# Kernel optimization log

Measured on AMD Instinct MI355X. Metric: run time of the kernel, lower is better.

The kernel has to match this reference:

```python
import jax, jax.numpy as jnp
import numpy as np

N_QUBITS = 13
DEPTH = 4
DIM = 2 ** N_QUBITS
PI = 3.141592653589793

# qubit 0 = most significant bit of the basis-state index
_idx = np.arange(DIM)
BITS = np.stack([(_idx >> (N_QUBITS - 1 - q)) & 1 for q in range(N_QUBITS)], axis=1)  # (DIM, n)
SIGNS = jnp.asarray(1.0 - 2.0 * BITS, dtype=jnp.float32)                               # Z eigenvalues, (DIM, n)
PARITY = jnp.asarray((-1.0) ** BITS.sum(axis=1), dtype=jnp.float32)                    # <Z^{(x)n}> diagonal, (DIM,)
# CZ entangling chain (q, q+1): diagonal (-1)^{sum_q b_q b_{q+1}}
ENT = jnp.asarray((-1.0) ** (BITS[:, :-1] * BITS[:, 1:]).sum(axis=1), dtype=jnp.float32)


def fwht(psi):
    """Normalized fast Walsh-Hadamard transform (H on every qubit), psi: (B, DIM) complex."""
    B = psi.shape[0]
    for q in range(N_QUBITS):
        psi = psi.reshape(B, 2 ** q, 2, -1)
        psi = jnp.stack([psi[:, :, 0] + psi[:, :, 1], psi[:, :, 0] - psi[:, :, 1]], axis=2)
    return psi.reshape(B, DIM) * (2.0 ** (-N_QUBITS / 2))


def feature_map_state(x):
    """Havlicek ZZ feature map: psi = D(x) H^n D(x) H^n |0...0>.
    Diagonal phase per basis state b: sum_j x_j s_j(b) + sum_{j<k} (pi-x_j)(pi-x_k) s_j(b) s_k(b)."""
    a = PI - x                                              # (B, n)
    u = x @ SIGNS.T                                         # (B, DIM)
    v = a @ SIGNS.T                                         # (B, DIM)
    phi = u + 0.5 * (v * v - jnp.sum(a * a, axis=1, keepdims=True))  # pair term via (sum)^2 trick
    d = jnp.exp(1j * phi)                                   # complex64 diagonal
    psi = jnp.full((x.shape[0], DIM), DIM ** -0.5, dtype=jnp.complex64)  # H^n |0>
    psi = fwht(d * psi)
    return d * psi


def _apply_1q(psi, U, q):
    """Apply 2x2 complex gate U to qubit q (bit-sliced)."""
    B = psi.shape[0]
    psi = psi.reshape(B, 2 ** q, 2, -1)
    a0, a1 = psi[:, :, 0], psi[:, :, 1]
    out = jnp.stack([U[0, 0] * a0 + U[0, 1] * a1, U[1, 0] * a0 + U[1, 1] * a1], axis=2)
    return out.reshape(B, DIM)


def variational_apply(psi, theta):
    """(DEPTH+1) layers of per-qubit Rz(b)Ry(a), CZ-chain entanglers between layers."""
    th = theta.reshape(DEPTH + 1, N_QUBITS, 2)
    for l in range(DEPTH + 1):
        if l > 0:
            psi = psi * ENT
        for q in range(N_QUBITS):
            ca = jnp.cos(0.5 * th[l, q, 0])
            sa = jnp.sin(0.5 * th[l, q, 0])
            em = jnp.exp(-0.5j * th[l, q, 1])
            ep = jnp.exp(0.5j * th[l, q, 1])
            U = jnp.stack([jnp.stack([em * ca, -em * sa]), jnp.stack([ep * sa, ep * ca])])
            psi = _apply_1q(psi, U, q)
    return psi


def setup_inputs() -> dict:
    key = jax.random.key(0)
    k1, k2 = jax.random.split(key)
    x = jax.random.normal(k1, (512, N_QUBITS), dtype=jnp.float32)
    theta = 0.1 * jax.random.normal(k2, ((DEPTH + 1) * N_QUBITS * 2,), dtype=jnp.float32)
    bias = jnp.zeros((1,), dtype=jnp.float32)
    return {"x": x, "theta": theta, "bias": bias}


def reference(x, theta, bias):
    psi = feature_map_state(x)
    psi = variational_apply(psi, theta)
    prob = psi.real ** 2 + psi.imag ** 2              # (B, DIM)
    logit = prob @ PARITY + bias[0]                   # (B,)
    return jnp.stack([-logit, logit], axis=1)         # two-class logits
```

## Files before the change

### kernel.cpp

```cpp
#include <hip/hip_runtime.h>
#include <hip/hip_fp16.h>

#define NQ   13
#define DIM  8192
#define PI_F 3.14159265358979323846f
#define NT   256
#define NAMP 32

__device__ __forceinline__ int lslot(int i) { return i + 4 * (i >> 5); }
#define NSLOT (DIM + 4 * (DIM >> 5))

__device__ __forceinline__ int base0(int t) { return 36 * t; }
__device__ __forceinline__ int base2(int t, int g) { return 1152 * g + 4 * t + 4 * (t >> 3); }
__device__ __forceinline__ int slot1(int t, int j) { return 1152 * (t >> 5) + 36 * j + (t & 31); }

union F4H { float4 f; __half2 h[4]; };

__device__ __forceinline__ void rsincos(float x, float* s, float* c) {
  const float INV2PI = 0.15915494309189535f;
  const float TWOPI  = 6.283185307179586f;
  float r = x * INV2PI;
  r -= rintf(r);
  float ang = r * TWOPI;
  *s = __sinf(ang);
  *c = __cosf(ang);
}

__device__ __forceinline__ void waveFence() {
  __builtin_amdgcn_wave_barrier();
  __threadfence_block();
  __builtin_amdgcn_wave_barrier();
}

__device__ __forceinline__ float2 f2fma(float s, float2 a, float2 b) {
  return make_float2(fmaf(s, a.x, b.x), fmaf(s, a.y, b.y));
}
__device__ __forceinline__ float2 f2add(float2 a, float2 b) {
  return make_float2(a.x + b.x, a.y + b.y);
}
__device__ __forceinline__ float2 f2sub(float2 a, float2 b) {
  return make_float2(a.x - b.x, a.y - b.y);
}
__device__ __forceinline__ float2 cphase(float2 v, float cs, float sn) {
  return make_float2(fmaf(cs, v.x, -sn * v.y), fmaf(cs, v.y, sn * v.x));
}
__device__ __forceinline__ float2 cmul(float2 a, float2 b) {
  return make_float2(fmaf(a.x, b.x, -a.y * b.y), fmaf(a.x, b.y, a.y * b.x));
}

template<int PAT>
__device__ __forceinline__ int ampIndex(int t, int j) {
  if constexpr (PAT == 0) return (t << 5) | j;
  else if constexpr (PAT == 1) return ((t >> 5) << 10) | (j << 5) | (t & 31);
  else return ((j >> 2) << 10) | (t << 2) | (j & 3);
}

template<int PAT>
__device__ __forceinline__ void buildTree(const float* __restrict__ w, float bias,
                                          int t, float* s) {
  float base = bias;
  if constexpr (PAT == 0) {
    #pragma unroll
    for (int k = 0; k < 8; k++) base += ((t >> k) & 1) ? w[5 + k] : 0.0f;
  } else {
    #pragma unroll
    for (int k = 0; k < 8; k++) base += ((t >> k) & 1) ? w[2 + k] : 0.0f;
  }
  constexpr int P[5] = { 0, 1,
                         (PAT == 0) ? 2 : 10,
                         (PAT == 0) ? 3 : 11,
                         (PAT == 0) ? 4 : 12 };
  s[0] = base;
  #pragma unroll
  for (int k = 0; k < 5; k++) {
    float wp = w[P[k]];
    #pragma unroll
    for (int m = 0; m < (1 << k); m++) s[m | (1 << k)] = s[m] + wp;
  }
}

__device__ __forceinline__ void loadA0f(const __half2* __restrict__ sAmp, int t, float2* amp) {
  const __half2* p = sAmp + base0(t);
  #pragma unroll
  for (int k = 0; k < 8; k++) {
    F4H u; u.f = *reinterpret_cast<const float4*>(p + 4 * k);
    #pragma unroll
    for (int c = 0; c < 4; c++) amp[4 * k + c] = __half22float2(u.h[c]);
  }
}
__device__ __forceinline__ void storeA0f(__half2* __restrict__ sAmp, int t, const float2* amp) {
  __half2* p = sAmp + base0(t);
  #pragma unroll
  for (int k = 0; k < 8; k++) {
    F4H u;
    #pragma unroll
    for (int c = 0; c < 4; c++) u.h[c] = __float22half2_rn(amp[4 * k + c]);
    *reinterpret_cast<float4*>(p + 4 * k) = u.f;
  }
}
__device__ __forceinline__ void loadA2f(const __half2* __restrict__ sAmp, int t, float2* amp) {
  #pragma unroll
  for (int g = 0; g < 8; g++) {
    F4H u; u.f = *reinterpret_cast<const float4*>(sAmp + base2(t, g));
    #pragma unroll
    for (int c = 0; c < 4; c++) amp[4 * g + c] = __half22float2(u.h[c]);
  }
}
__device__ __forceinline__ void storeA2f(__half2* __restrict__ sAmp, int t, const float2* amp) {
  #pragma unroll
  for (int g = 0; g < 8; g++) {
    F4H u;
    #pragma unroll
    for (int c = 0; c < 4; c++) u.h[c] = __float22half2_rn(amp[4 * g + c]);
    *reinterpret_cast<float4*>(sAmp + base2(t, g)) = u.f;
  }
}

__device__ __forceinline__ void loadA0h(const __half2* __restrict__ sAmp, int t, __half2* amp) {
  const __half2* p = sAmp + base0(t);
  #pragma unroll
  for (int k = 0; k < 8; k++) {
    F4H u; u.f = *reinterpret_cast<const float4*>(p + 4 * k);
    #pragma unroll
    for (int c = 0; c < 4; c++) amp[4 * k + c] = u.h[c];
  }
}
__device__ __forceinline__ void storeA0h(__half2* __restrict__ sAmp, int t, const __half2* amp) {
  __half2* p = sAmp + base0(t);
  #pragma unroll
  for (int k = 0; k < 8; k++) {
    F4H u;
    #pragma unroll
    for (int c = 0; c < 4; c++) u.h[c] = amp[4 * k + c];
    *reinterpret_cast<float4*>(p + 4 * k) = u.f;
  }
}
__device__ __forceinline__ void loadA1h(const __half2* __restrict__ sAmp, int t, __half2* amp) {
  #pragma unroll
  for (int j = 0; j < NAMP; j++) amp[j] = sAmp[slot1(t, j)];
}
__device__ __forceinline__ void storeA1h(__half2* __restrict__ sAmp, int t, const __half2* amp) {
  #pragma unroll
  for (int j = 0; j < NAMP; j++) sAmp[slot1(t, j)] = amp[j];
}

template<int KB>
__device__ __forceinline__ void fwht_bit(float2* amp) {
  #pragma unroll
  for (int j = 0; j < NAMP; j++) if (!(j & (1 << KB))) {
    int j1 = j | (1 << KB);
    float2 a0 = amp[j], a1 = amp[j1];
    amp[j]  = f2add(a0, a1);
    amp[j1] = f2sub(a0, a1);
  }
}
template<int KB>
__device__ __forceinline__ void applyRy(float2* amp, float ta, float sa) {
  #pragma unroll
  for (int j = 0; j < NAMP; j++) if (!(j & (1 << KB))) {
    int j1 = j | (1 << KB);
    amp[j]  = f2fma(-ta, amp[j1], amp[j]);
    amp[j1] = f2fma( sa, amp[j],  amp[j1]);
    amp[j]  = f2fma(-ta, amp[j1], amp[j]);
  }
}

template<int KB>
__device__ __forceinline__ void fwht_bitH(__half2* amp) {
  #pragma unroll
  for (int j = 0; j < NAMP; j++) if (!(j & (1 << KB))) {
    int j1 = j | (1 << KB);
    __half2 a0 = amp[j], a1 = amp[j1];
    amp[j]  = __hadd2(a0, a1);
    amp[j1] = __hsub2(a0, a1);
  }
}
template<int KB>
__device__ __forceinline__ void applyRyH(__half2* amp, __half2 nta, __half2 sa) {
  #pragma unroll
  for (int j = 0; j < NAMP; j++) if (!(j & (1 << KB))) {
    int j1 = j | (1 << KB);
    amp[j]  = __hfma2(nta, amp[j1], amp[j]);
    amp[j1] = __hfma2(sa,  amp[j],  amp[j1]);
    amp[j]  = __hfma2(nta, amp[j1], amp[j]);
  }
}

template<int PAT, bool INIT>
__device__ __forceinline__ void featureDiag(float2* amp,
                                            const float* __restrict__ wX,
                                            const float* __restrict__ wA,
                                            const float* __restrict__ cons, int t) {
  float u[NAMP], v[NAMP];
  buildTree<PAT>(wX, cons[0], t, u);
  buildTree<PAT>(wA, cons[1], t, v);
  float A2 = cons[2];
  #pragma unroll
  for (int j = 0; j < NAMP; j++) {
    float phi = u[j] + 0.5f * (v[j] * v[j] - A2);
    float sn, cs; rsincos(phi, &sn, &cs);
    if constexpr (INIT) amp[j] = make_float2(cs, sn);
    else                amp[j] = cphase(amp[j], cs, sn);
  }
}

__device__ __forceinline__ void applyDiagPT2(float2* amp,
                                             const float* __restrict__ wb,
                                             const float* __restrict__ eR,
                                             const float* __restrict__ eI,
                                             float bias, int t) {
  float base = bias;
  #pragma unroll
  for (int k = 0; k < 8; k++) base += ((t >> k) & 1) ? wb[2 + k] : 0.0f;
  float2 c[16];
  { float sn, cs; rsincos(base, &sn, &cs); c[0] = make_float2(cs, sn); }
  constexpr int EB[4] = {0, 1, 10, 11};
  #pragma unroll
  for (int k = 0; k < 4; k++) {
    float2 e = make_float2(eR[EB[k]], eI[EB[k]]);
    #pragma unroll
    for (int m = 0; m < (1 << k); m++) c[m | (1 << k)] = cmul(c[m], e);
  }
  #pragma unroll
  for (int j = 0; j < 16; j++) {
    int i = ampIndex<2>(t, j);
    float sgn = (__popc(i & (i >> 1)) & 1) ? -1.0f : 1.0f;
    amp[j] = cphase(amp[j], c[j].x * sgn, c[j].y * sgn);
  }
  float2 e4 = make_float2(eR[12], eI[12]);
  #pragma unroll
  for (int j = 16; j < 32; j++) {
    int i = ampIndex<2>(t, j);
    float sgn = (__popc(i & (i >> 1)) & 1) ? -1.0f : 1.0f;
    float2 cc = cmul(c[j - 16], e4);
    amp[j] = cphase(amp[j], cc.x * sgn, cc.y * sgn);
  }
}

__global__ __launch_bounds__(NT, 1) void qc_kernel(
    const float* __restrict__ xin,
    const float* __restrict__ thin,
    const float* __restrict__ bin,
    float* __restrict__ out) {
  __shared__ alignas(16) __half2 sAmp[NSLOT];
  __shared__ float gTA[65], gSA[65];
  __shared__ __half2 hNTA[65], hSA[65];
  __shared__ float gBbit[65];
  __shared__ float eBr[65], eBi[65];
  __shared__ float wX[13], wA[13];
  __shared__ float cons[8];
  __shared__ float red[NT / 64];

  const int t = threadIdx.x;
  const int b = blockIdx.x;

  if (t < NQ) {
    float xq = xin[b * NQ + t];
    float aq = PI_F - xq;
    wX[12 - t] = -2.0f * xq;
    wA[12 - t] = -2.0f * aq;
  }
  if (t < 65) {
    float av = thin[2 * t];
    float bv = thin[2 * t + 1];
    float ca = cosf(0.5f * av);
    float sa = sinf(0.5f * av);
    float ta = sa / (1.0f + ca);
    gTA[t] = ta;
    gSA[t] = sa;
    hNTA[t] = __float2half2_rn(-ta);
    hSA[t]  = __float2half2_rn(sa);
    int l = t / NQ, q = t % NQ;
    int s = l * NQ + (12 - q);
    gBbit[s] = bv;
    eBr[s] = cosf(bv);
    eBi[s] = sinf(bv);
  }
  __syncthreads();
  if (t == 0) {
    float X = 0.f, A = 0.f, A2 = 0.f;
    for (int p = 0; p < NQ; p++) {
      float xq = -0.5f * wX[p], aq = -0.5f * wA[p];
      X += xq; A += aq; A2 += aq * aq;
    }
    cons[0] = X; cons[1] = A; cons[2] = A2;
    for (int l = 0; l < 5; l++) {
      float s = 0.f;
      for (int p = 0; p < NQ; p++) s += gBbit[l * NQ + p];
      cons[3 + l] = -0.5f * s;
    }
  }
  __syncthreads();

  {
    float2 amp[NAMP];
    featureDiag<0, true>(amp, wX, wA, cons, t);
    fwht_bit<0>(amp); fwht_bit<1>(amp); fwht_bit<2>(amp);
    fwht_bit<3>(amp); fwht_bit<4>(amp);
    storeA0f(sAmp, t, amp);
  }
  waveFence();

  {
    __half2 amp[NAMP];
    loadA1h(sAmp, t, amp);
    fwht_bitH<0>(amp); fwht_bitH<1>(amp); fwht_bitH<2>(amp);
    fwht_bitH<3>(amp); fwht_bitH<4>(amp);
    storeA1h(sAmp, t, amp);
  }
  __syncthreads();

  {
    float2 amp[NAMP];
    loadA2f(sAmp, t, amp);
    fwht_bit<2>(amp); fwht_bit<3>(amp); fwht_bit<4>(amp);
    featureDiag<2, false>(amp, wX, wA, cons, t);
    applyRy<0>(amp, gTA[12], gSA[12]);
    applyRy<1>(amp, gTA[11], gSA[11]);
    applyRy<2>(amp, gTA[2],  gSA[2]);
    applyRy<3>(amp, gTA[1],  gSA[1]);
    applyRy<4>(amp, gTA[0],  gSA[0]);
    storeA2f(sAmp, t, amp);
  }
  __syncthreads();

  float acc = 0.0f;
  for (int l = 0; l < 5; l++) {
    const int g = l * NQ;
    {
      __half2 amp[NAMP];
      loadA0h(sAmp, t, amp);
      applyRyH<2>(amp, hNTA[g + 10], hSA[g + 10]);
      applyRyH<3>(amp, hNTA[g + 9],  hSA[g + 9]);
      applyRyH<4>(amp, hNTA[g + 8],  hSA[g + 8]);
      storeA0h(sAmp, t, amp);
    }
    waveFence();
    {
      __half2 amp[NAMP];
      loadA1h(sAmp, t, amp);
      applyRyH<0>(amp, hNTA[g + 7], hSA[g + 7]);
      applyRyH<1>(amp, hNTA[g + 6], hSA[g + 6]);
      applyRyH<2>(amp, hNTA[g + 5], hSA[g + 5]);
      applyRyH<3>(amp, hNTA[g + 4], hSA[g + 4]);
      applyRyH<4>(amp, hNTA[g + 3], hSA[g + 3]);
      if (l < 4) {
        storeA1h(sAmp, t, amp);
      } else {
        #pragma unroll
        for (int j = 0; j < NAMP; j++) {
          int i = ampIndex<1>(t, j);
          float2 a = __half22float2(amp[j]);
          float p2 = fmaf(a.x, a.x, a.y * a.y);
          acc += (__popc(i) & 1) ? -p2 : p2;
        }
      }
    }
    if (l < 4) {
      __syncthreads();
      const int g1 = (l + 1) * NQ;
      float2 amp[NAMP];
      loadA2f(sAmp, t, amp);
      applyDiagPT2(amp, gBbit + l * NQ, eBr + l * NQ, eBi + l * NQ,
                   cons[3 + l], t);
      applyRy<0>(amp, gTA[g1 + 12], gSA[g1 + 12]);
      applyRy<1>(amp, gTA[g1 + 11], gSA[g1 + 11]);
      applyRy<2>(amp, gTA[g1 + 2],  gSA[g1 + 2]);
      applyRy<3>(amp, gTA[g1 + 1],  gSA[g1 + 1]);
      applyRy<4>(amp, gTA[g1 + 0],  gSA[g1 + 0]);
      storeA2f(sAmp, t, amp);
      __syncthreads();
    }
  }

  #pragma unroll
  for (int off = 32; off > 0; off >>= 1) acc += __shfl_down(acc, off, 64);
  if ((t & 63) == 0) red[t >> 6] = acc;
  __syncthreads();
  if (t == 0) {
    float total = red[0] + red[1] + red[2] + red[3];
    float logit = total * (1.0f / 67108864.0f) + bin[0];
    out[b * 2 + 0] = -logit;
    out[b * 2 + 1] = logit;
  }
}

extern "C" void kernel_launch(void* const* d_in, const int* in_sizes, int n_in,
                              void* d_out, int out_size, void* d_ws, size_t ws_size,
                              hipStream_t stream) {
  const float* x  = (const float*)d_in[0];
  const float* th = (const float*)d_in[1];
  const float* bi = (const float*)d_in[2];
  float* out = (float*)d_out;
  int B = in_sizes[0] / NQ;
  qc_kernel<<<B, NT, 0, stream>>>(x, th, bi, out);
}
```

Baseline: 90.17 us.

## Use 512 threads with 16 amplitudes each and re-plan shared-memory passes

Doubles the block to 512 threads, with each thread holding 16 amplitudes instead of 32. This cuts register pressure and lets launch bounds request more resident blocks. The 13-qubit state is now split into 4-bit passes with new padded shared-memory layouts, a new two-half load pattern, and a rearranged gate and diagonal order. Each layer now needs more shared-memory round trips and block barriers, which adds sync and LDS traffic in exchange for higher occupancy.

New measurement: 90.47 us. Within noise of the previous version (+0.3%).

```diff
diff --git a/kernel.cpp b/kernel.cpp
--- a/kernel.cpp
+++ b/kernel.cpp
@@ -4,15 +4,19 @@
 #define NQ   13
 #define DIM  8192
 #define PI_F 3.14159265358979323846f
-#define NT   256
-#define NAMP 32
-
-__device__ __forceinline__ int lslot(int i) { return i + 4 * (i >> 5); }
-#define NSLOT (DIM + 4 * (DIM >> 5))
-
-__device__ __forceinline__ int base0(int t) { return 36 * t; }
-__device__ __forceinline__ int base2(int t, int g) { return 1152 * g + 4 * t + 4 * (t >> 3); }
-__device__ __forceinline__ int slot1(int t, int j) { return 1152 * (t >> 5) + 36 * j + (t & 31); }
+#define NT   512
+#define NAMP 16
+
+#define NSLOT 9712
+
+__device__ __forceinline__ int base0(int t) { return 16 * t + 4 * (t >> 1) + 16 * (t >> 4); }
+__device__ __forceinline__ int slot1f(int t, int j) {
+  return 304 * (t >> 4) + (t & 15) + 16 * j + 4 * (j >> 1);
+}
+__device__ __forceinline__ int slot2f(int t, int j) {
+  return 4864 * (t >> 8) + (t & 255) + 4 * ((t >> 5) & 7) + 304 * j;
+}
+__device__ __forceinline__ int base3(int t) { return 8 * t + 4 * (t >> 2) + 16 * (t >> 5); }
 
 union F4H { float4 f; __half2 h[4]; };
 
@@ -48,41 +52,10 @@
   return make_float2(fmaf(a.x, b.x, -a.y * b.y), fmaf(a.x, b.y, a.y * b.x));
 }
 
-template<int PAT>
-__device__ __forceinline__ int ampIndex(int t, int j) {
-  if constexpr (PAT == 0) return (t << 5) | j;
-  else if constexpr (PAT == 1) return ((t >> 5) << 10) | (j << 5) | (t & 31);
-  else return ((j >> 2) << 10) | (t << 2) | (j & 3);
-}
-
-template<int PAT>
-__device__ __forceinline__ void buildTree(const float* __restrict__ w, float bias,
-                                          int t, float* s) {
-  float base = bias;
-  if constexpr (PAT == 0) {
-    #pragma unroll
-    for (int k = 0; k < 8; k++) base += ((t >> k) & 1) ? w[5 + k] : 0.0f;
-  } else {
-    #pragma unroll
-    for (int k = 0; k < 8; k++) base += ((t >> k) & 1) ? w[2 + k] : 0.0f;
-  }
-  constexpr int P[5] = { 0, 1,
-                         (PAT == 0) ? 2 : 10,
-                         (PAT == 0) ? 3 : 11,
-                         (PAT == 0) ? 4 : 12 };
-  s[0] = base;
-  #pragma unroll
-  for (int k = 0; k < 5; k++) {
-    float wp = w[P[k]];
-    #pragma unroll
-    for (int m = 0; m < (1 << k); m++) s[m | (1 << k)] = s[m] + wp;
-  }
-}
-
 __device__ __forceinline__ void loadA0f(const __half2* __restrict__ sAmp, int t, float2* amp) {
   const __half2* p = sAmp + base0(t);
   #pragma unroll
-  for (int k = 0; k < 8; k++) {
+  for (int k = 0; k < 4; k++) {
     F4H u; u.f = *reinterpret_cast<const float4*>(p + 4 * k);
     #pragma unroll
     for (int c = 0; c < 4; c++) amp[4 * k + c] = __half22float2(u.h[c]);
@@ -91,57 +64,72 @@
 __device__ __forceinline__ void storeA0f(__half2* __restrict__ sAmp, int t, const float2* amp) {
   __half2* p = sAmp + base0(t);
   #pragma unroll
-  for (int k = 0; k < 8; k++) {
+  for (int k = 0; k < 4; k++) {
     F4H u;
     #pragma unroll
     for (int c = 0; c < 4; c++) u.h[c] = __float22half2_rn(amp[4 * k + c]);
     *reinterpret_cast<float4*>(p + 4 * k) = u.f;
   }
 }
+
+__device__ __forceinline__ void loadA3f(const __half2* __restrict__ sAmp, int t, float2* amp) {
+  const __half2* p = sAmp + base3(t);
+  #pragma unroll
+  for (int k = 0; k < 2; k++) {
+    F4H u; u.f = *reinterpret_cast<const float4*>(p + 4 * k);
+    #pragma unroll
+    for (int c = 0; c < 4; c++) amp[4 * k + c] = __half22float2(u.h[c]);
+  }
+  p += 4864;
+  #pragma unroll
+  for (int k = 0; k < 2; k++) {
+    F4H u; u.f = *reinterpret_cast<const float4*>(p + 4 * k);
+    #pragma unroll
+    for (int c = 0; c < 4; c++) amp[8 + 4 * k + c] = __half22float2(u.h[c]);
+  }
+}
+__device__ __forceinline__ void storeA3f(__half2* __restrict__ sAmp, int t, const float2* amp) {
+  __half2* p = sAmp + base3(t);
+  #pragma unroll
+  for (int k = 0; k < 2; k++) {
+    F4H u;
+    #pragma unroll
+    for (int c = 0; c < 4; c++) u.h[c] = __float22half2_rn(amp[4 * k + c]);
+    *reinterpret_cast<float4*>(p + 4 * k) = u.f;
+  }
+  p += 4864;
+  #pragma unroll
+  for (int k = 0; k < 2; k++) {
+    F4H u;
+    #pragma unroll
+    for (int c = 0; c < 4; c++) u.h[c] = __float22half2_rn(amp[8 + 4 * k + c]);
+    *reinterpret_cast<float4*>(p + 4 * k) = u.f;
+  }
+}
+
+__device__ __forceinline__ void loadA1h(const __half2* __restrict__ sAmp, int t, __half2* amp) {
+  #pragma unroll
+  for (int j = 0; j < NAMP; j++) amp[j] = sAmp[slot1f(t, j)];
+}
+__device__ __forceinline__ void storeA1h(__half2* __restrict__ sAmp, int t, const __half2* amp) {
+  #pragma unroll
+  for (int j = 0; j < NAMP; j++) sAmp[slot1f(t, j)] = amp[j];
+}
+__device__ __forceinline__ void loadA2h(const __half2* __restrict__ sAmp, int t, __half2* amp) {
+  #pragma unroll
+  for (int j = 0; j < NAMP; j++) amp[j] = sAmp[slot2f(t, j)];
+}
+__device__ __forceinline__ void storeA2h(__half2* __restrict__ sAmp, int t, const __half2* amp) {
+  #pragma unroll
+  for (int j = 0; j < NAMP; j++) sAmp[slot2f(t, j)] = amp[j];
+}
 __device__ __forceinline__ void loadA2f(const __half2* __restrict__ sAmp, int t, float2* amp) {
   #pragma unroll
-  for (int g = 0; g < 8; g++) {
-    F4H u; u.f = *reinterpret_cast<const float4*>(sAmp + base2(t, g));
-    #pragma unroll
-    for (int c = 0; c < 4; c++) amp[4 * g + c] = __half22float2(u.h[c]);
-  }
+  for (int j = 0; j < NAMP; j++) amp[j] = __half22float2(sAmp[slot2f(t, j)]);
 }
 __device__ __forceinline__ void storeA2f(__half2* __restrict__ sAmp, int t, const float2* amp) {
   #pragma unroll
-  for (int g = 0; g < 8; g++) {
-    F4H u;
-    #pragma unroll
-    for (int c = 0; c < 4; c++) u.h[c] = __float22half2_rn(amp[4 * g + c]);
-    *reinterpret_cast<float4*>(sAmp + base2(t, g)) = u.f;
-  }
-}
-
-__device__ __forceinline__ void loadA0h(const __half2* __restrict__ sAmp, int t, __half2* amp) {
-  const __half2* p = sAmp + base0(t);
-  #pragma unroll
-  for (int k = 0; k < 8; k++) {
-    F4H u; u.f = *reinterpret_cast<const float4*>(p + 4 * k);
-    #pragma unroll
-    for (int c = 0; c < 4; c++) amp[4 * k + c] = u.h[c];
-  }
-}
-__device__ __forceinline__ void storeA0h(__half2* __restrict__ sAmp, int t, const __half2* amp) {
-  __half2* p = sAmp + base0(t);
-  #pragma unroll
-  for (int k = 0; k < 8; k++) {
-    F4H u;
-    #pragma unroll
-    for (int c = 0; c < 4; c++) u.h[c] = amp[4 * k + c];
-    *reinterpret_cast<float4*>(p + 4 * k) = u.f;
-  }
-}
-__device__ __forceinline__ void loadA1h(const __half2* __restrict__ sAmp, int t, __half2* amp) {
-  #pragma unroll
-  for (int j = 0; j < NAMP; j++) amp[j] = sAmp[slot1(t, j)];
-}
-__device__ __forceinline__ void storeA1h(__half2* __restrict__ sAmp, int t, const __half2* amp) {
-  #pragma unroll
-  for (int j = 0; j < NAMP; j++) sAmp[slot1(t, j)] = amp[j];
+  for (int j = 0; j < NAMP; j++) sAmp[slot2f(t, j)] = __float22half2_rn(amp[j]);
 }
 
 template<int KB>
@@ -183,6 +171,23 @@
     amp[j]  = __hfma2(nta, amp[j1], amp[j]);
     amp[j1] = __hfma2(sa,  amp[j],  amp[j1]);
     amp[j]  = __hfma2(nta, amp[j1], amp[j]);
+  }
+}
+
+template<int PAT>
+__device__ __forceinline__ void buildTree(const float* __restrict__ w, float bias,
+                                          int t, float* s) {
+  float base = bias;
+  constexpr int B0 = (PAT == 0) ? 4 : 3;
+  #pragma unroll
+  for (int k = 0; k < 9; k++) base += ((t >> k) & 1) ? w[B0 + k] : 0.0f;
+  constexpr int P[4] = { 0, 1, 2, (PAT == 0) ? 3 : 12 };
+  s[0] = base;
+  #pragma unroll
+  for (int k = 0; k < 4; k++) {
+    float wp = w[P[k]];
+    #pragma unroll
+    for (int m = 0; m < (1 << k); m++) s[m | (1 << k)] = s[m] + wp;
   }
 }
 
@@ -204,40 +209,31 @@
   }
 }
 
-__device__ __forceinline__ void applyDiagPT2(float2* amp,
-                                             const float* __restrict__ wb,
-                                             const float* __restrict__ eR,
-                                             const float* __restrict__ eI,
-                                             float bias, int t) {
+__device__ __forceinline__ void applyDiagW0(float2* amp,
+                                            const float* __restrict__ wb,
+                                            const float* __restrict__ eR,
+                                            const float* __restrict__ eI,
+                                            float bias, int t) {
   float base = bias;
   #pragma unroll
-  for (int k = 0; k < 8; k++) base += ((t >> k) & 1) ? wb[2 + k] : 0.0f;
+  for (int k = 0; k < 9; k++) base += ((t >> k) & 1) ? wb[4 + k] : 0.0f;
   float2 c[16];
   { float sn, cs; rsincos(base, &sn, &cs); c[0] = make_float2(cs, sn); }
-  constexpr int EB[4] = {0, 1, 10, 11};
   #pragma unroll
   for (int k = 0; k < 4; k++) {
-    float2 e = make_float2(eR[EB[k]], eI[EB[k]]);
+    float2 e = make_float2(eR[k], eI[k]);
     #pragma unroll
     for (int m = 0; m < (1 << k); m++) c[m | (1 << k)] = cmul(c[m], e);
   }
   #pragma unroll
   for (int j = 0; j < 16; j++) {
-    int i = ampIndex<2>(t, j);
+    int i = (t << 4) | j;
     float sgn = (__popc(i & (i >> 1)) & 1) ? -1.0f : 1.0f;
     amp[j] = cphase(amp[j], c[j].x * sgn, c[j].y * sgn);
   }
-  float2 e4 = make_float2(eR[12], eI[12]);
-  #pragma unroll
-  for (int j = 16; j < 32; j++) {
-    int i = ampIndex<2>(t, j);
-    float sgn = (__popc(i & (i >> 1)) & 1) ? -1.0f : 1.0f;
-    float2 cc = cmul(c[j - 16], e4);
-    amp[j] = cphase(amp[j], cc.x * sgn, cc.y * sgn);
-  }
-}
-
-__global__ __launch_bounds__(NT, 1) void qc_kernel(
+}
+
+__global__ __launch_bounds__(NT, 4) void qc_kernel(
     const float* __restrict__ xin,
     const float* __restrict__ thin,
     const float* __restrict__ bin,
@@ -295,8 +291,7 @@
   {
     float2 amp[NAMP];
     featureDiag<0, true>(amp, wX, wA, cons, t);
-    fwht_bit<0>(amp); fwht_bit<1>(amp); fwht_bit<2>(amp);
-    fwht_bit<3>(amp); fwht_bit<4>(amp);
+    fwht_bit<0>(amp); fwht_bit<1>(amp); fwht_bit<2>(amp); fwht_bit<3>(amp);
     storeA0f(sAmp, t, amp);
   }
   waveFence();
@@ -304,8 +299,7 @@
   {
     __half2 amp[NAMP];
     loadA1h(sAmp, t, amp);
-    fwht_bitH<0>(amp); fwht_bitH<1>(amp); fwht_bitH<2>(amp);
-    fwht_bitH<3>(amp); fwht_bitH<4>(amp);
+    fwht_bitH<0>(amp); fwht_bitH<1>(amp); fwht_bitH<2>(amp); fwht_bitH<3>(amp);
     storeA1h(sAmp, t, amp);
   }
   __syncthreads();
@@ -313,64 +307,74 @@
   {
     float2 amp[NAMP];
     loadA2f(sAmp, t, amp);
-    fwht_bit<2>(amp); fwht_bit<3>(amp); fwht_bit<4>(amp);
-    featureDiag<2, false>(amp, wX, wA, cons, t);
+    fwht_bit<0>(amp); fwht_bit<1>(amp); fwht_bit<2>(amp); fwht_bit<3>(amp);
+    storeA2f(sAmp, t, amp);
+  }
+  __syncthreads();
+
+  {
+    float2 amp[NAMP];
+    loadA3f(sAmp, t, amp);
+    fwht_bit<3>(amp);
+    featureDiag<3, false>(amp, wX, wA, cons, t);
     applyRy<0>(amp, gTA[12], gSA[12]);
     applyRy<1>(amp, gTA[11], gSA[11]);
-    applyRy<2>(amp, gTA[2],  gSA[2]);
-    applyRy<3>(amp, gTA[1],  gSA[1]);
-    applyRy<4>(amp, gTA[0],  gSA[0]);
-    storeA2f(sAmp, t, amp);
+    applyRy<2>(amp, gTA[10], gSA[10]);
+    applyRy<3>(amp, gTA[0],  gSA[0]);
+    storeA3f(sAmp, t, amp);
   }
   __syncthreads();
 
   float acc = 0.0f;
   for (int l = 0; l < 5; l++) {
     const int g = l * NQ;
+    if (l > 0) {
+      float2 amp[NAMP];
+      loadA3f(sAmp, t, amp);
+      applyRy<0>(amp, gTA[g + 12], gSA[g + 12]);
+      applyRy<1>(amp, gTA[g + 11], gSA[g + 11]);
+      applyRy<2>(amp, gTA[g + 10], gSA[g + 10]);
+      applyRy<3>(amp, gTA[g + 0],  gSA[g + 0]);
+      storeA3f(sAmp, t, amp);
+      __syncthreads();
+    }
     {
       __half2 amp[NAMP];
-      loadA0h(sAmp, t, amp);
-      applyRyH<2>(amp, hNTA[g + 10], hSA[g + 10]);
-      applyRyH<3>(amp, hNTA[g + 9],  hSA[g + 9]);
-      applyRyH<4>(amp, hNTA[g + 8],  hSA[g + 8]);
-      storeA0h(sAmp, t, amp);
-    }
-    waveFence();
+      loadA2h(sAmp, t, amp);
+      applyRyH<0>(amp, hNTA[g + 4], hSA[g + 4]);
+      applyRyH<1>(amp, hNTA[g + 3], hSA[g + 3]);
+      applyRyH<2>(amp, hNTA[g + 2], hSA[g + 2]);
+      applyRyH<3>(amp, hNTA[g + 1], hSA[g + 1]);
+      storeA2h(sAmp, t, amp);
+    }
+    __syncthreads();
     {
       __half2 amp[NAMP];
       loadA1h(sAmp, t, amp);
-      applyRyH<0>(amp, hNTA[g + 7], hSA[g + 7]);
-      applyRyH<1>(amp, hNTA[g + 6], hSA[g + 6]);
-      applyRyH<2>(amp, hNTA[g + 5], hSA[g + 5]);
-      applyRyH<3>(amp, hNTA[g + 4], hSA[g + 4]);
-      applyRyH<4>(amp, hNTA[g + 3], hSA[g + 3]);
+      applyRyH<0>(amp, hNTA[g + 8], hSA[g + 8]);
+      applyRyH<1>(amp, hNTA[g + 7], hSA[g + 7]);
+      applyRyH<2>(amp, hNTA[g + 6], hSA[g + 6]);
+      applyRyH<3>(amp, hNTA[g + 5], hSA[g + 5]);
+      storeA1h(sAmp, t, amp);
+    }
+    waveFence();
+    {
+      float2 amp[NAMP];
+      loadA0f(sAmp, t, amp);
+      applyRy<3>(amp, gTA[g + 9], gSA[g + 9]);
       if (l < 4) {
-        storeA1h(sAmp, t, amp);
+        applyDiagW0(amp, gBbit + g, eBr + g, eBi + g, cons[3 + l], t);
+        storeA0f(sAmp, t, amp);
       } else {
+        int pt = __popc(t) & 1;
         #pragma unroll
         for (int j = 0; j < NAMP; j++) {
-          int i = ampIndex<1>(t, j);
-          float2 a = __half22float2(amp[j]);
-          float p2 = fmaf(a.x, a.x, a.y * a.y);
-          acc += (__popc(i) & 1) ? -p2 : p2;
+          float p2 = fmaf(amp[j].x, amp[j].x, amp[j].y * amp[j].y);
+          acc += ((pt + __popc(j)) & 1) ? -p2 : p2;
         }
       }
     }
-    if (l < 4) {
-      __syncthreads();
-      const int g1 = (l + 1) * NQ;
-      float2 amp[NAMP];
-      loadA2f(sAmp, t, amp);
-      applyDiagPT2(amp, gBbit + l * NQ, eBr + l * NQ, eBi + l * NQ,
-                   cons[3 + l], t);
-      applyRy<0>(amp, gTA[g1 + 12], gSA[g1 + 12]);
-      applyRy<1>(amp, gTA[g1 + 11], gSA[g1 + 11]);
-      applyRy<2>(amp, gTA[g1 + 2],  gSA[g1 + 2]);
-      applyRy<3>(amp, gTA[g1 + 1],  gSA[g1 + 1]);
-      applyRy<4>(amp, gTA[g1 + 0],  gSA[g1 + 0]);
-      storeA2f(sAmp, t, amp);
-      __syncthreads();
-    }
+    if (l < 4) __syncthreads();
   }
 
   #pragma unroll
@@ -378,7 +382,9 @@
   if ((t & 63) == 0) red[t >> 6] = acc;
   __syncthreads();
   if (t == 0) {
-    float total = red[0] + red[1] + red[2] + red[3];
+    float total = 0.f;
+    #pragma unroll
+    for (int w = 0; w < NT / 64; w++) total += red[w];
     float logit = total * (1.0f / 67108864.0f) + bin[0];
     out[b * 2 + 0] = -logit;
     out[b * 2 + 1] = logit;
```
